# Kernel tuning notes

Measured on AMD Instinct MI355X. Metric: run time of the kernel, lower is better.

## Reference

```python
import jax, jax.numpy as jnp
import numpy as np

N_OPENIE = 100000
N_ENTITY = 100000
E = 150000
D_IN = 512
D_OUT = 512
H = 8
DH = D_OUT // H
NEG_SLOPE = 0.2


def setup_inputs() -> dict:
    key = jax.random.key(0)
    ks = jax.random.split(key, 16)
    def rn(k, shape, scale=0.05):
        return jax.random.normal(k, shape, dtype=jnp.float32) * scale
    return {
        "x_openie": jax.random.normal(ks[0], (N_OPENIE, D_IN), dtype=jnp.float32),
        "x_entity": jax.random.normal(ks[1], (N_ENTITY, D_IN), dtype=jnp.float32),
        "edge_e2o": jax.random.randint(ks[2], (2, E), 0, N_OPENIE, dtype=jnp.int32),
        "edge_o2o": jax.random.randint(ks[3], (2, E), 0, N_OPENIE, dtype=jnp.int32),
        "proj_o_w": rn(ks[4], (D_IN, D_OUT)),
        "proj_o_b": jnp.zeros((D_OUT,), jnp.float32),
        "proj_e_w": rn(ks[5], (D_IN, D_OUT)),
        "proj_e_b": jnp.zeros((D_OUT,), jnp.float32),
        "att_src_e2o": rn(ks[6], (H, DH)),
        "att_dst_e2o": rn(ks[7], (H, DH)),
        "att_src_o2o": rn(ks[8], (H, DH)),
        "att_dst_o2o": rn(ks[9], (H, DH)),
        "k_lin_w": rn(ks[10], (D_OUT, D_OUT)),
        "k_lin_b": jnp.zeros((D_OUT,), jnp.float32),
        "q_sem": rn(ks[11], (D_OUT,)),
        "lin_w": rn(ks[12], (D_OUT, 2)),
        "lin_b": jnp.zeros((2,), jnp.float32),
    }


def _edge_type_conv(h_src, h_dst, att_src, att_dst, src, dst, n_dst):
    # GAT-style per-edge-type attention (one metapath of HANConv).
    a_src = jnp.einsum('nhd,hd->nh', h_src, att_src)  # [N_src, H]
    a_dst = jnp.einsum('nhd,hd->nh', h_dst, att_dst)  # [N_dst, H]
    alpha = jax.nn.leaky_relu(a_src[src] + a_dst[dst], NEG_SLOPE)  # [E, H]
    amax = jax.ops.segment_max(alpha, dst, num_segments=n_dst)     # [N_dst, H]
    ex = jnp.exp(alpha - amax[dst])
    denom = jax.ops.segment_sum(ex, dst, num_segments=n_dst)
    w = ex / (denom[dst] + 1e-16)                                   # softmax over in-edges
    msg = h_src[src] * w[:, :, None]                                # [E, H, DH]
    out = jax.ops.segment_sum(msg, dst, num_segments=n_dst)        # [N_dst, H, DH]
    return jax.nn.relu(out.reshape(n_dst, H * DH))


def reference(x_openie, x_entity, edge_e2o, edge_o2o, proj_o_w, proj_o_b, proj_e_w,
              proj_e_b, att_src_e2o, att_dst_e2o, att_src_o2o, att_dst_o2o,
              k_lin_w, k_lin_b, q_sem, lin_w, lin_b):
    # Per-node-type projection to heads
    h_o = (x_openie @ proj_o_w + proj_o_b).reshape(-1, H, DH)
    h_e = (x_entity @ proj_e_w + proj_e_b).reshape(-1, H, DH)
    # Two metapaths ending at 'openie'
    out0 = _edge_type_conv(h_e, h_o, att_src_e2o, att_dst_e2o, edge_e2o[0], edge_e2o[1], N_OPENIE)
    out1 = _edge_type_conv(h_o, h_o, att_src_o2o, att_dst_o2o, edge_o2o[0], edge_o2o[1], N_OPENIE)
    # Semantic-level attention across metapaths
    outs = jnp.stack([out0, out1])                         # [M, N, F]
    k = jnp.tanh(outs @ k_lin_w + k_lin_b).mean(axis=1)    # [M, F]
    sem = jax.nn.softmax((k * q_sem).sum(-1))              # [M]
    fused = jnp.einsum('m,mnf->nf', sem, outs)             # [N, F]
    # global mean pool (single graph) -> dropout (eval: identity) -> Linear(F, 2)
    pooled = fused.mean(axis=0, keepdims=True)             # [1, F]
    return pooled @ lin_w + lin_b                          # [1, 2]
```

## Files before the change

### kernel.cpp

```cpp
#include <hip/hip_runtime.h>
#include <math.h>

#define N_NODES 100000
#define N_EDGES 150000
#define D 512
#define H 8
#define NEG_SLOPE 0.2f
#define NBR 782
#define NBLK (NBR * 4)

typedef __attribute__((ext_vector_type(8))) short bf16x8;
typedef __attribute__((ext_vector_type(4))) float f32x4;

__device__ __forceinline__ float bf2f(unsigned short u) { return __uint_as_float(((unsigned int)u) << 16); }
__device__ __forceinline__ unsigned short f2bf(float f) {
    unsigned int u = __float_as_uint(f);
    unsigned int r = u + 0x7FFFu + ((u >> 16) & 1u);
    return (unsigned short)(r >> 16);
}
__device__ __forceinline__ unsigned int pkbf(float a, float b) {
    unsigned int ua = __float_as_uint(a) + 0x8000u;
    unsigned int ub = __float_as_uint(b) + 0x8000u;
    return (ua >> 16) | (ub & 0xFFFF0000u);
}
__device__ __forceinline__ void gl_lds16(const void* g, void* l) {
    __builtin_amdgcn_global_load_lds((const __attribute__((address_space(1))) void*)g,
                                     (__attribute__((address_space(3))) void*)l, 16, 0, 0);
}
__device__ __forceinline__ float fast_tanh(float x) {
    float e = __expf(2.0f * x);
    float r;
    asm("v_rcp_f32 %0, %1" : "=v"(r) : "v"(e + 1.0f));
    return 1.0f - 2.0f * r;
}
__device__ __forceinline__ void map_block(int lin, int& rblk, int& cblk) {
    int g = lin >> 5;
    if (g < (NBR >> 3)) { rblk = g * 8 + (lin & 7); cblk = (lin >> 3) & 3; }
    else { int idx = lin - (NBR >> 3) * 32; rblk = (NBR & ~7) + (idx >> 2); cblk = idx & 3; }
}

__global__ __launch_bounds__(256)
void hist_edges(const int* __restrict__ e2o, const int* __restrict__ o2o, int* __restrict__ deg) {
    int i = blockIdx.x * 256 + threadIdx.x;
    if (i < N_EDGES) atomicAdd(&deg[e2o[N_EDGES + i]], 1);
    else if (i < 2 * N_EDGES) atomicAdd(&deg[N_NODES + o2o[N_EDGES + (i - N_EDGES)]], 1);
}

__global__ __launch_bounds__(256)
void scan1(const int* __restrict__ deg, int* __restrict__ rowptr, int* __restrict__ partials, int n) {
    __shared__ int lds[256];
    int t = threadIdx.x, b = blockIdx.x;
    int base = b * 1024 + t * 4;
    int d0 = (base + 0 < n) ? deg[base + 0] : 0;
    int d1 = (base + 1 < n) ? deg[base + 1] : 0;
    int d2 = (base + 2 < n) ? deg[base + 2] : 0;
    int d3 = (base + 3 < n) ? deg[base + 3] : 0;
    int s = d0 + d1 + d2 + d3;
    lds[t] = s;
    __syncthreads();
    for (int off = 1; off < 256; off <<= 1) {
        int v = (t >= off) ? lds[t - off] : 0;
        __syncthreads();
        lds[t] += v;
        __syncthreads();
    }
    int incl = lds[t];
    int eb = incl - s;
    if (base + 0 < n) rowptr[base + 0] = eb;
    if (base + 1 < n) rowptr[base + 1] = eb + d0;
    if (base + 2 < n) rowptr[base + 2] = eb + d0 + d1;
    if (base + 3 < n) rowptr[base + 3] = eb + d0 + d1 + d2;
    if (t == 255) partials[b] = incl;
}

__global__ __launch_bounds__(256)
void scan23(int* __restrict__ rowptr, const int* __restrict__ partials,
            int* __restrict__ cursor, int n, int total, int nb) {
    __shared__ int lds[256];
    int t = threadIdx.x, b = blockIdx.x;
    lds[t] = (t < nb) ? partials[t] : 0;
    __syncthreads();
    for (int off = 1; off < 256; off <<= 1) {
        int v = (t >= off) ? lds[t - off] : 0;
        __syncthreads();
        lds[t] += v;
        __syncthreads();
    }
    int add = (b == 0) ? 0 : lds[b - 1];
    int base = b * 1024 + t * 4;
    #pragma unroll
    for (int j = 0; j < 4; ++j) {
        if (base + j < n) {
            int v = rowptr[base + j] + add;
            rowptr[base + j] = v;
            cursor[base + j] = v;
        }
    }
    if (b == 0 && t == 0) rowptr[n] = total;
}

__global__ __launch_bounds__(256)
void fill_csr(const int* __restrict__ e2o, const int* __restrict__ o2o,
              int* __restrict__ cursor, int* __restrict__ csr) {
    int i = blockIdx.x * 256 + threadIdx.x;
    if (i < N_EDGES) {
        int d = e2o[N_EDGES + i];
        int p = atomicAdd(&cursor[d], 1);
        csr[p] = e2o[i];
    } else if (i < 2 * N_EDGES) {
        int j = i - N_EDGES;
        int d = o2o[N_EDGES + j];
        int p = atomicAdd(&cursor[N_NODES + d], 1);
        csr[p] = o2o[j];
    }
}

__global__ __launch_bounds__(256)
void transpose3(const float* __restrict__ W0, const float* __restrict__ W1, const float* __restrict__ W2,
                unsigned short* __restrict__ T0, unsigned short* __restrict__ T1, unsigned short* __restrict__ T2) {
    __shared__ float tile[32][33];
    int z = blockIdx.z;
    const float* W = (z == 0) ? W0 : (z == 1) ? W1 : W2;
    unsigned short* T = (z == 0) ? T0 : (z == 1) ? T1 : T2;
    int bx = blockIdx.x, by = blockIdx.y;
    int t = threadIdx.x, tx = t & 31, ty = t >> 5;
    #pragma unroll
    for (int p = 0; p < 4; ++p) {
        int k = by * 32 + ty + p * 8;
        tile[ty + p * 8][tx] = W[(size_t)k * D + bx * 32 + tx];
    }
    __syncthreads();
    #pragma unroll
    for (int p = 0; p < 4; ++p) {
        int n = bx * 32 + ty + p * 8;
        T[(size_t)n * D + by * 32 + tx] = f2bf(tile[tx][ty + p * 8]);
    }
}

__global__ __launch_bounds__(256)
void convert2(const float4* __restrict__ x0, const float4* __restrict__ x1,
              uint2* __restrict__ y0, uint2* __restrict__ y1) {
    const int n4 = N_NODES * D / 4;
    int i = blockIdx.x * 256 + threadIdx.x;
    const float4* s; uint2* d; int j;
    if (i < n4) { s = x0; d = y0; j = i; }
    else { s = x1; d = y1; j = i - n4; }
    float4 v = s[j];
    uint2 o; o.x = pkbf(v.x, v.y); o.y = pkbf(v.z, v.w);
    d[j] = o;
}

__global__ __launch_bounds__(256)
void gemm_proj2(const unsigned short* __restrict__ A0, const unsigned short* __restrict__ A1,
                const unsigned short* __restrict__ Bt0, const unsigned short* __restrict__ Bt1,
                const float* __restrict__ b0, const float* __restrict__ b1,
                unsigned short* __restrict__ C0, unsigned short* __restrict__ C1,
                const float* __restrict__ at00, const float* __restrict__ at01, const float* __restrict__ at02,
                float* __restrict__ ao00, float* __restrict__ ao01, float* __restrict__ ao02,
                const float* __restrict__ at10, float* __restrict__ ao10)
{
    __shared__ __align__(16) unsigned short As[2][4096];
    __shared__ __align__(16) unsigned short Bs[2][4096];
    const int M = N_NODES;
    int lin = blockIdx.x;
    int half = (lin >= NBLK) ? 1 : 0;
    lin -= half * NBLK;
    int rblk, cblk; map_block(lin, rblk, cblk);
    const unsigned short* A  = half ? A1 : A0;
    const unsigned short* Bt = half ? Bt1 : Bt0;
    const float* bias        = half ? b1 : b0;
    unsigned short* C        = half ? C1 : C0;
    const int natt = half ? 1 : 3;
    const float* attA = half ? at10 : at00;
    const float* attB = at01;
    const float* attC = at02;
    float* aoA = half ? ao10 : ao00;
    float* aoB = ao01;
    float* aoC = ao02;

    const int tid = threadIdx.x, lane = tid & 63, wave = tid >> 6;
    const int rb = rblk * 128, cb = cblk * 128;
    const int wm = (wave >> 1) * 64, wn = (wave & 1) * 64;

    const unsigned short* agp[2]; const unsigned short* bgp[2];
    #pragma unroll
    for (int c = 0; c < 2; ++c) {
        int s = wave * 2 + c;
        int rA = rb + s * 16 + (lane & 15); if (rA > M - 1) rA = M - 1;
        agp[c] = A + (size_t)rA * D + (lane >> 4) * 8;
        int rB = cb + s * 16 + (lane & 15);
        bgp[c] = Bt + (size_t)rB * D + (lane >> 4) * 8;
    }

    f32x4 acc[4][4];
    #pragma unroll
    for (int i = 0; i < 4; ++i)
        #pragma unroll
        for (int j = 0; j < 4; ++j) acc[i][j] = (f32x4){0.f, 0.f, 0.f, 0.f};

    #pragma unroll
    for (int c = 0; c < 2; ++c) {
        int s = wave * 2 + c;
        gl_lds16(agp[c], &As[0][s * 512]); agp[c] += 32;
        gl_lds16(bgp[c], &Bs[0][s * 512]); bgp[c] += 32;
    }
    __syncthreads();

    int buf = 0;
    for (int k = 0; k < 16; ++k) {
        if (k < 15) {
            #pragma unroll
            for (int c = 0; c < 2; ++c) {
                int s = wave * 2 + c;
                gl_lds16(agp[c], &As[buf ^ 1][s * 512]); agp[c] += 32;
                gl_lds16(bgp[c], &Bs[buf ^ 1][s * 512]); bgp[c] += 32;
            }
        }
        bf16x8 af[4], bfr[4];
        #pragma unroll
        for (int mi = 0; mi < 4; ++mi) af[mi] = *(const bf16x8*)&As[buf][((wave >> 1) * 4 + mi) * 512 + lane * 8];
        #pragma unroll
        for (int ni = 0; ni < 4; ++ni) bfr[ni] = *(const bf16x8*)&Bs[buf][((wave & 1) * 4 + ni) * 512 + lane * 8];
        #pragma unroll
        for (int mi = 0; mi < 4; ++mi)
            #pragma unroll
            for (int ni = 0; ni < 4; ++ni)
                acc[mi][ni] = __builtin_amdgcn_mfma_f32_16x16x32_bf16(af[mi], bfr[ni], acc[mi][ni], 0, 0, 0);
        __syncthreads();
        buf ^= 1;
    }

    float bb[4], av0[4], av1[4], av2[4];
    const int head = (cb + wn) >> 6;
    #pragma unroll
    for (int ni = 0; ni < 4; ++ni) {
        int ci = ni * 16 + (lane & 15);
        bb[ni] = bias[cb + wn + ci];
        av0[ni] = attA[head * 64 + ci];
        if (natt > 1) { av1[ni] = attB[head * 64 + ci]; av2[ni] = attC[head * 64 + ci]; }
    }
    #pragma unroll
    for (int mi = 0; mi < 4; ++mi) {
        #pragma unroll
        for (int r = 0; r < 4; ++r) {
            int rg = rb + wm + mi * 16 + (lane >> 4) * 4 + r;
            bool ok = rg < M;
            float v[4];
            #pragma unroll
            for (int ni = 0; ni < 4; ++ni) v[ni] = acc[mi][ni][r] + bb[ni];
            if (ok) {
                size_t base = (size_t)rg * D + cb + wn + (lane & 15);
                #pragma unroll
                for (int ni = 0; ni < 4; ++ni) C[base + ni * 16] = f2bf(v[ni]);
            }
            float s0 = v[0] * av0[0] + v[1] * av0[1] + v[2] * av0[2] + v[3] * av0[3];
            float s1 = 0.f, s2 = 0.f;
            if (natt > 1) {
                s1 = v[0] * av1[0] + v[1] * av1[1] + v[2] * av1[2] + v[3] * av1[3];
                s2 = v[0] * av2[0] + v[1] * av2[1] + v[2] * av2[2] + v[3] * av2[3];
            }
            #pragma unroll
            for (int m2 = 1; m2 < 16; m2 <<= 1) {
                s0 += __shfl_xor(s0, m2);
                if (natt > 1) { s1 += __shfl_xor(s1, m2); s2 += __shfl_xor(s2, m2); }
            }
            if (ok && (lane & 15) == 0) {
                aoA[rg * H + head] = s0;
                if (natt > 1) { aoB[rg * H + head] = s1; aoC[rg * H + head] = s2; }
            }
        }
    }
}

__global__ __launch_bounds__(256)
void aggregate2(const int* __restrict__ rowptr, const int* __restrict__ csr,
                const float* __restrict__ aS0, const float* __restrict__ aD0, const unsigned short* __restrict__ hE,
                const float* __restrict__ aS1, const float* __restrict__ aD1, const unsigned short* __restrict__ hO,
                unsigned short* __restrict__ out0, unsigned short* __restrict__ out1)
{
    int gw = (blockIdx.x * 256 + threadIdx.x) >> 6;
    int lane = threadIdx.x & 63;
    if (gw >= 2 * N_NODES) return;
    int half = gw >= N_NODES;
    int node = gw - half * N_NODES;
    const float* a_src = half ? aS1 : aS0;
    const float* a_dst = half ? aD1 : aD0;
    const unsigned short* h = half ? hO : hE;
    unsigned short* out = half ? out1 : out0;

    int beg = rowptr[gw], end = rowptr[gw + 1];
    int hh = lane & 7;
    float adst = a_dst[node * H + hh];

    float amax = -1e30f;
    for (int p = beg; p < end; ++p) {
        int s = csr[p];
        float al = a_src[s * H + hh] + adst;
        al = (al >= 0.f) ? al : NEG_SLOPE * al;
        amax = fmaxf(amax, al);
    }
    float denom = 0.f;
    for (int p = beg; p < end; ++p) {
        int s = csr[p];
        float al = a_src[s * H + hh] + adst;
        al = (al >= 0.f) ? al : NEG_SLOPE * al;
        denom += expf(al - amax);
    }
    float inv = 1.f / (denom + 1e-16f);

    float acc[8] = {0.f, 0.f, 0.f, 0.f, 0.f, 0.f, 0.f, 0.f};
    for (int p = beg; p < end; ++p) {
        int s = csr[p];
        float al = a_src[s * H + hh] + adst;
        al = (al >= 0.f) ? al : NEG_SLOPE * al;
        float w = expf(al - amax) * inv;
        const unsigned short* hp = h + (size_t)s * D;
        #pragma unroll
        for (int h2 = 0; h2 < 8; ++h2) {
            float wh = __shfl(w, h2);
            acc[h2] += bf2f(hp[h2 * 64 + lane]) * wh;
        }
    }
    size_t base = (size_t)node * D;
    #pragma unroll
    for (int h2 = 0; h2 < 8; ++h2)
        out[base + h2 * 64 + lane] = f2bf(fmaxf(acc[h2], 0.f));
}

__global__ __launch_bounds__(256)
void colsum2(const unsigned short* __restrict__ ob0, const unsigned short* __restrict__ ob1,
             float* __restrict__ colsum)
{
    __shared__ float red[512];
    int b = blockIdx.x;
    int half = b >= NBR;
    const unsigned short* ob = half ? ob1 : ob0;
    float* cs = colsum + half * 512;
    int t = threadIdx.x;
    int r0 = (b - half * NBR) * 128;
    int c8 = t & 63;
    float s[8] = {0.f, 0.f, 0.f, 0.f, 0.f, 0.f, 0.f, 0.f};
    for (int it = 0; it < 32; ++it) {
        int row = r0 + it * 4 + (t >> 6);
        if (row < N_NODES) {
            uint4 v = *((const uint4*)(ob + (size_t)row * D) + c8);
            s[0] += bf2f((unsigned short)(v.x & 0xFFFF)); s[1] += bf2f((unsigned short)(v.x >> 16));
            s[2] += bf2f((unsigned short)(v.y & 0xFFFF)); s[3] += bf2f((unsigned short)(v.y >> 16));
            s[4] += bf2f((unsigned short)(v.z & 0xFFFF)); s[5] += bf2f((unsigned short)(v.z >> 16));
            s[6] += bf2f((unsigned short)(v.w & 0xFFFF)); s[7] += bf2f((unsigned short)(v.w >> 16));
        }
    }
    red[t] = 0.f; red[t + 256] = 0.f;
    __syncthreads();
    #pragma unroll
    for (int j = 0; j < 8; ++j) atomicAdd(&red[c8 * 8 + j], s[j]);
    __syncthreads();
    atomicAdd(&cs[t & 511], red[t]);
    atomicAdd(&cs[(t + 256) & 511], red[t + 256]);
}

__global__ __launch_bounds__(256)
void gemm_tanh2(const unsigned short* __restrict__ Ah0, const unsigned short* __restrict__ Ah1,
                const unsigned short* __restrict__ Bt, const float* __restrict__ bias,
                float* __restrict__ ksum)
{
    __shared__ __align__(16) unsigned short As[2][4096];
    __shared__ __align__(16) unsigned short Bs[2][4096];
    const int M = N_NODES;
    int lin = blockIdx.x;
    int half = (lin >= NBLK) ? 1 : 0;
    lin -= half * NBLK;
    int rblk, cblk; map_block(lin, rblk, cblk);
    const unsigned short* A = half ? Ah1 : Ah0;
    float* ks = ksum + half * 512;

    const int tid = threadIdx.x, lane = tid & 63, wave = tid >> 6;
    const int rb = rblk * 128, cb = cblk * 128;
    const int wm = (wave >> 1) * 64, wn = (wave & 1) * 64;

    const unsigned short* agp[2]; const unsigned short* bgp[2];
    #pragma unroll
    for (int c = 0; c < 2; ++c) {
        int s = wave * 2 + c;
        int rA = rb + s * 16 + (lane & 15); if (rA > M - 1) rA = M - 1;
        agp[c] = A + (size_t)rA * D + (lane >> 4) * 8;
        int rB = cb + s * 16 + (lane & 15);
        bgp[c] = Bt + (size_t)rB * D + (lane >> 4) * 8;
    }

    f32x4 acc[4][4];
    #pragma unroll
    for (int i = 0; i < 4; ++i)
        #pragma unroll
        for (int j = 0; j < 4; ++j) acc[i][j] = (f32x4){0.f, 0.f, 0.f, 0.f};

    #pragma unroll
    for (int c = 0; c < 2; ++c) {
        int s = wave * 2 + c;
        gl_lds16(agp[c], &As[0][s * 512]); agp[c] += 32;
        gl_lds16(bgp[c], &Bs[0][s * 512]); bgp[c] += 32;
    }
    __syncthreads();

    int buf = 0;
    for (int k = 0; k < 16; ++k) {
        if (k < 15) {
            #pragma unroll
            for (int c = 0; c < 2; ++c) {
                int s = wave * 2 + c;
                gl_lds16(agp[c], &As[buf ^ 1][s * 512]); agp[c] += 32;
                gl_lds16(bgp[c], &Bs[buf ^ 1][s * 512]); bgp[c] += 32;
            }
        }
        bf16x8 af[4], bfr[4];
        #pragma unroll
        for (int mi = 0; mi < 4; ++mi) af[mi] = *(const bf16x8*)&As[buf][((wave >> 1) * 4 + mi) * 512 + lane * 8];
        #pragma unroll
        for (int ni = 0; ni < 4; ++ni) bfr[ni] = *(const bf16x8*)&Bs[buf][((wave & 1) * 4 + ni) * 512 + lane * 8];
        #pragma unroll
        for (int mi = 0; mi < 4; ++mi)
            #pragma unroll
            for (int ni = 0; ni < 4; ++ni)
                acc[mi][ni] = __builtin_amdgcn_mfma_f32_16x16x32_bf16(af[mi], bfr[ni], acc[mi][ni], 0, 0, 0);
        __syncthreads();
        buf ^= 1;
    }

    float bb[4];
    #pragma unroll
    for (int ni = 0; ni < 4; ++ni) bb[ni] = bias[cb + wn + ni * 16 + (lane & 15)];
    float cs[4] = {0.f, 0.f, 0.f, 0.f};
    #pragma unroll
    for (int mi = 0; mi < 4; ++mi) {
        #pragma unroll
        for (int r = 0; r < 4; ++r) {
            int rg = rb + wm + mi * 16 + (lane >> 4) * 4 + r;
            if (rg < M) {
                #pragma unroll
                for (int ni = 0; ni < 4; ++ni)
                    cs[ni] += fast_tanh(acc[mi][ni][r] + bb[ni]);
            }
        }
    }
    __syncthreads();
    float* red = (float*)As;
    if (tid < 128) red[tid] = 0.f;
    __syncthreads();
    #pragma unroll
    for (int ni = 0; ni < 4; ++ni) atomicAdd(&red[wn + ni * 16 + (lane & 15)], cs[ni]);
    __syncthreads();
    if (tid < 128) atomicAdd(&ks[cb + tid], red[tid]);
}

__global__ __launch_bounds__(256)
void finalize(const float* __restrict__ ksum, const float* __restrict__ colsum,
              const float* __restrict__ q_sem, const float* __restrict__ lin_w,
              const float* __restrict__ lin_b, float* __restrict__ dout)
{
    __shared__ float red[256];
    __shared__ float semsh[2];
    int t = threadIdx.x;
    const float invN = 1.0f / (float)N_NODES;
    float p0 = ksum[t] * q_sem[t] + ksum[t + 256] * q_sem[t + 256];
    float p1 = ksum[512 + t] * q_sem[t] + ksum[512 + t + 256] * q_sem[t + 256];

    red[t] = p0; __syncthreads();
    for (int s = 128; s > 0; s >>= 1) { if (t < s) red[t] += red[t + s]; __syncthreads(); }
    float S0 = red[0]; __syncthreads();
    red[t] = p1; __syncthreads();
    for (int s = 128; s > 0; s >>= 1) { if (t < s) red[t] += red[t + s]; __syncthreads(); }
    float S1 = red[0]; __syncthreads();

    if (t == 0) {
        float a0 = S0 * invN, a1 = S1 * invN;
        float mx = fmaxf(a0, a1);
        float e0 = expf(a0 - mx), e1 = expf(a1 - mx);
        semsh[0] = e0 / (e0 + e1);
        semsh[1] = e1 / (e0 + e1);
    }
    __syncthreads();
    float sem0 = semsh[0], sem1 = semsh[1];

    float o0 = 0.f, o1 = 0.f;
    #pragma unroll
    for (int q = 0; q < 2; ++q) {
        int f = t + q * 256;
        float pooled = (sem0 * colsum[f] + sem1 * colsum[512 + f]) * invN;
        o0 += pooled * lin_w[f * 2 + 0];
        o1 += pooled * lin_w[f * 2 + 1];
    }
    red[t] = o0; __syncthreads();
    for (int s = 128; s > 0; s >>= 1) { if (t < s) red[t] += red[t + s]; __syncthreads(); }
    if (t == 0) dout[0] = red[0] + lin_b[0];
    __syncthreads();
    red[t] = o1; __syncthreads();
    for (int s = 128; s > 0; s >>= 1) { if (t < s) red[t] += red[t + s]; __syncthreads(); }
    if (t == 0) dout[1] = red[0] + lin_b[1];
}

extern "C" void kernel_launch(void* const* d_in, const int* in_sizes, int n_in,
                              void* d_out, int out_size, void* d_ws, size_t ws_size,
                              hipStream_t stream)
{
    const float* x_o    = (const float*)d_in[0];
    const float* x_e    = (const float*)d_in[1];
    const int*   e2o    = (const int*)d_in[2];
    const int*   o2o    = (const int*)d_in[3];
    const float* pow_   = (const float*)d_in[4];
    const float* pob    = (const float*)d_in[5];
    const float* pew    = (const float*)d_in[6];
    const float* peb    = (const float*)d_in[7];
    const float* as_e2o = (const float*)d_in[8];
    const float* ad_e2o = (const float*)d_in[9];
    const float* as_o2o = (const float*)d_in[10];
    const float* ad_o2o = (const float*)d_in[11];
    const float* klw    = (const float*)d_in[12];
    const float* klb    = (const float*)d_in[13];
    const float* qsem   = (const float*)d_in[14];
    const float* linw   = (const float*)d_in[15];
    const float* linb   = (const float*)d_in[16];

    char* ws = (char*)d_ws;
    size_t off = 0;
    auto alloc = [&](size_t bytes) { void* p = ws + off; off += (bytes + 255) & ~(size_t)255; return p; };

    unsigned short* xbf_o = (unsigned short*)alloc((size_t)N_NODES * D * 2);
    unsigned short* xbf_e = (unsigned short*)alloc((size_t)N_NODES * D * 2);
    unsigned short* h_o   = (unsigned short*)alloc((size_t)N_NODES * D * 2);
    unsigned short* h_e   = (unsigned short*)alloc((size_t)N_NODES * D * 2);
    unsigned short* obf0  = (unsigned short*)alloc((size_t)N_NODES * D * 2);
    unsigned short* obf1  = (unsigned short*)alloc((size_t)N_NODES * D * 2);
    unsigned short* wt_po = (unsigned short*)alloc((size_t)D * D * 2);
    unsigned short* wt_pe = (unsigned short*)alloc((size_t)D * D * 2);
    unsigned short* wt_kl = (unsigned short*)alloc((size_t)D * D * 2);
    float* aS0 = (float*)alloc((size_t)N_NODES * H * 4);
    float* aD0 = (float*)alloc((size_t)N_NODES * H * 4);
    float* aS1 = (float*)alloc((size_t)N_NODES * H * 4);
    float* aD1 = (float*)alloc((size_t)N_NODES * H * 4);
    int* misc    = (int*)alloc((2048 + 2 * N_NODES) * 4);
    float* colsum = (float*)misc;
    float* ksum   = colsum + 1024;
    int* deg      = misc + 2048;
    int* cursor  = (int*)alloc(2 * N_NODES * 4);
    int* rowptr  = (int*)alloc((2 * N_NODES + 1) * 4);
    int* partials= (int*)alloc(256 * 4);
    int* csr     = (int*)alloc(2 * N_EDGES * 4);

    const int NSC = 2 * N_NODES;
    const int NB1 = (NSC + 1023) / 1024;
    const int EH  = (2 * N_EDGES + 255) / 256;

    hipMemsetAsync(misc, 0, (size_t)(2048 + 2 * N_NODES) * 4, stream);

    hist_edges<<<EH, 256, 0, stream>>>(e2o, o2o, deg);
    scan1<<<NB1, 256, 0, stream>>>(deg, rowptr, partials, NSC);
    scan23<<<NB1, 256, 0, stream>>>(rowptr, partials, cursor, NSC, 2 * N_EDGES, NB1);
    fill_csr<<<EH, 256, 0, stream>>>(e2o, o2o, cursor, csr);

    transpose3<<<dim3(16, 16, 3), 256, 0, stream>>>(pow_, pew, klw, wt_po, wt_pe, wt_kl);
    convert2<<<(2 * N_NODES * D / 4) / 256, 256, 0, stream>>>(
        (const float4*)x_o, (const float4*)x_e, (uint2*)xbf_o, (uint2*)xbf_e);

    gemm_proj2<<<2 * NBLK, 256, 0, stream>>>(
        xbf_o, xbf_e, wt_po, wt_pe, pob, peb, h_o, h_e,
        ad_e2o, as_o2o, ad_o2o, aD0, aS1, aD1,
        as_e2o, aS0);

    aggregate2<<<(2 * N_NODES * 64) / 256, 256, 0, stream>>>(
        rowptr, csr, aS0, aD0, h_e, aS1, aD1, h_o, obf0, obf1);
    colsum2<<<2 * NBR, 256, 0, stream>>>(obf0, obf1, colsum);
    gemm_tanh2<<<2 * NBLK, 256, 0, stream>>>(obf0, obf1, wt_kl, klb, ksum);

    finalize<<<1, 256, 0, stream>>>(ksum, colsum, qsem, linw, linb, (float*)d_out);
}
```

Baseline: 1.211 ms.

## Triple-buffer LDS in projection and tanh GEMMs with partial vmcnt waits

Both bf16 MFMA GEMM kernels move from a double-buffered LDS pipeline to a three-stage ring, prefetching two K-tiles ahead. The full __syncthreads is replaced by explicit s_waitcnt vmcnt(4) plus s_barrier, so only the oldest tile's loads must complete. This is meant to hide global-load latency behind MFMA work. In exchange, LDS use per block grows from 32KB to 48KB, which may lower occupancy, and correctness now depends on hand-counted vmcnt values.

```diff
diff --git a/kernel.cpp b/kernel.cpp
--- a/kernel.cpp
+++ b/kernel.cpp
@@ -159,8 +159,8 @@
                 float* __restrict__ ao00, float* __restrict__ ao01, float* __restrict__ ao02,
                 const float* __restrict__ at10, float* __restrict__ ao10)
 {
-    __shared__ __align__(16) unsigned short As[2][4096];
-    __shared__ __align__(16) unsigned short Bs[2][4096];
+    __shared__ __align__(16) unsigned short As[3][4096];
+    __shared__ __align__(16) unsigned short Bs[3][4096];
     const int M = N_NODES;
     int lin = blockIdx.x;
     int half = (lin >= NBLK) ? 1 : 0;
@@ -183,9 +183,11 @@
     const int wm = (wave >> 1) * 64, wn = (wave & 1) * 64;
 
     const unsigned short* agp[2]; const unsigned short* bgp[2];
+    int sub[2];
     #pragma unroll
     for (int c = 0; c < 2; ++c) {
         int s = wave * 2 + c;
+        sub[c] = s;
         int rA = rb + s * 16 + (lane & 15); if (rA > M - 1) rA = M - 1;
         agp[c] = A + (size_t)rA * D + (lane >> 4) * 8;
         int rB = cb + s * 16 + (lane & 15);
@@ -200,34 +202,46 @@
 
     #pragma unroll
     for (int c = 0; c < 2; ++c) {
-        int s = wave * 2 + c;
-        gl_lds16(agp[c], &As[0][s * 512]); agp[c] += 32;
-        gl_lds16(bgp[c], &Bs[0][s * 512]); bgp[c] += 32;
-    }
-    __syncthreads();
-
-    int buf = 0;
+        gl_lds16(agp[c], &As[0][sub[c] * 512]); agp[c] += 32;
+        gl_lds16(bgp[c], &Bs[0][sub[c] * 512]); bgp[c] += 32;
+    }
+    #pragma unroll
+    for (int c = 0; c < 2; ++c) {
+        gl_lds16(agp[c], &As[1][sub[c] * 512]); agp[c] += 32;
+        gl_lds16(bgp[c], &Bs[1][sub[c] * 512]); bgp[c] += 32;
+    }
+    asm volatile("s_waitcnt vmcnt(4)" ::: "memory");
+    __builtin_amdgcn_s_barrier();
+
+    unsigned short *aR = As[0], *bR = Bs[0];
+    unsigned short *aM = As[1], *bM = Bs[1];
+    unsigned short *aP = As[2], *bP = Bs[2];
+
     for (int k = 0; k < 16; ++k) {
-        if (k < 15) {
+        bf16x8 af[4], bfr[4];
+        #pragma unroll
+        for (int mi = 0; mi < 4; ++mi) af[mi] = *(const bf16x8*)&aR[((wave >> 1) * 4 + mi) * 512 + lane * 8];
+        #pragma unroll
+        for (int ni = 0; ni < 4; ++ni) bfr[ni] = *(const bf16x8*)&bR[((wave & 1) * 4 + ni) * 512 + lane * 8];
+        if (k < 14) {
             #pragma unroll
             for (int c = 0; c < 2; ++c) {
-                int s = wave * 2 + c;
-                gl_lds16(agp[c], &As[buf ^ 1][s * 512]); agp[c] += 32;
-                gl_lds16(bgp[c], &Bs[buf ^ 1][s * 512]); bgp[c] += 32;
+                gl_lds16(agp[c], &aP[sub[c] * 512]); agp[c] += 32;
+                gl_lds16(bgp[c], &bP[sub[c] * 512]); bgp[c] += 32;
             }
         }
-        bf16x8 af[4], bfr[4];
-        #pragma unroll
-        for (int mi = 0; mi < 4; ++mi) af[mi] = *(const bf16x8*)&As[buf][((wave >> 1) * 4 + mi) * 512 + lane * 8];
-        #pragma unroll
-        for (int ni = 0; ni < 4; ++ni) bfr[ni] = *(const bf16x8*)&Bs[buf][((wave & 1) * 4 + ni) * 512 + lane * 8];
         #pragma unroll
         for (int mi = 0; mi < 4; ++mi)
             #pragma unroll
             for (int ni = 0; ni < 4; ++ni)
                 acc[mi][ni] = __builtin_amdgcn_mfma_f32_16x16x32_bf16(af[mi], bfr[ni], acc[mi][ni], 0, 0, 0);
-        __syncthreads();
-        buf ^= 1;
+        __builtin_amdgcn_sched_barrier(0);
+        if (k < 14) asm volatile("s_waitcnt vmcnt(4) lgkmcnt(0)" ::: "memory");
+        else        asm volatile("s_waitcnt vmcnt(0) lgkmcnt(0)" ::: "memory");
+        __builtin_amdgcn_s_barrier();
+        unsigned short* t;
+        t = aR; aR = aM; aM = aP; aP = t;
+        t = bR; bR = bM; bM = bP; bP = t;
     }
 
     float bb[4], av0[4], av1[4], av2[4];
@@ -364,8 +378,8 @@
                 const unsigned short* __restrict__ Bt, const float* __restrict__ bias,
                 float* __restrict__ ksum)
 {
-    __shared__ __align__(16) unsigned short As[2][4096];
-    __shared__ __align__(16) unsigned short Bs[2][4096];
+    __shared__ __align__(16) unsigned short As[3][4096];
+    __shared__ __align__(16) unsigned short Bs[3][4096];
     const int M = N_NODES;
     int lin = blockIdx.x;
     int half = (lin >= NBLK) ? 1 : 0;
@@ -379,9 +393,11 @@
     const int wm = (wave >> 1) * 64, wn = (wave & 1) * 64;
 
     const unsigned short* agp[2]; const unsigned short* bgp[2];
+    int sub[2];
     #pragma unroll
     for (int c = 0; c < 2; ++c) {
         int s = wave * 2 + c;
+        sub[c] = s;
         int rA = rb + s * 16 + (lane & 15); if (rA > M - 1) rA = M - 1;
         agp[c] = A + (size_t)rA * D + (lane >> 4) * 8;
         int rB = cb + s * 16 + (lane & 15);
@@ -396,34 +412,46 @@
 
     #pragma unroll
     for (int c = 0; c < 2; ++c) {
-        int s = wave * 2 + c;
-        gl_lds16(agp[c], &As[0][s * 512]); agp[c] += 32;
-        gl_lds16(bgp[c], &Bs[0][s * 512]); bgp[c] += 32;
-    }
-    __syncthreads();
-
-    int buf = 0;
+        gl_lds16(agp[c], &As[0][sub[c] * 512]); agp[c] += 32;
+        gl_lds16(bgp[c], &Bs[0][sub[c] * 512]); bgp[c] += 32;
+    }
+    #pragma unroll
+    for (int c = 0; c < 2; ++c) {
+        gl_lds16(agp[c], &As[1][sub[c] * 512]); agp[c] += 32;
+        gl_lds16(bgp[c], &Bs[1][sub[c] * 512]); bgp[c] += 32;
+    }
+    asm volatile("s_waitcnt vmcnt(4)" ::: "memory");
+    __builtin_amdgcn_s_barrier();
+
+    unsigned short *aR = As[0], *bR = Bs[0];
+    unsigned short *aM = As[1], *bM = Bs[1];
+    unsigned short *aP = As[2], *bP = Bs[2];
+
     for (int k = 0; k < 16; ++k) {
-        if (k < 15) {
+        bf16x8 af[4], bfr[4];
+        #pragma unroll
+        for (int mi = 0; mi < 4; ++mi) af[mi] = *(const bf16x8*)&aR[((wave >> 1) * 4 + mi) * 512 + lane * 8];
+        #pragma unroll
+        for (int ni = 0; ni < 4; ++ni) bfr[ni] = *(const bf16x8*)&bR[((wave & 1) * 4 + ni) * 512 + lane * 8];
+        if (k < 14) {
             #pragma unroll
             for (int c = 0; c < 2; ++c) {
-                int s = wave * 2 + c;
-                gl_lds16(agp[c], &As[buf ^ 1][s * 512]); agp[c] += 32;
-                gl_lds16(bgp[c], &Bs[buf ^ 1][s * 512]); bgp[c] += 32;
+                gl_lds16(agp[c], &aP[sub[c] * 512]); agp[c] += 32;
+                gl_lds16(bgp[c], &bP[sub[c] * 512]); bgp[c] += 32;
             }
         }
-        bf16x8 af[4], bfr[4];
-        #pragma unroll
-        for (int mi = 0; mi < 4; ++mi) af[mi] = *(const bf16x8*)&As[buf][((wave >> 1) * 4 + mi) * 512 + lane * 8];
-        #pragma unroll
-        for (int ni = 0; ni < 4; ++ni) bfr[ni] = *(const bf16x8*)&Bs[buf][((wave & 1) * 4 + ni) * 512 + lane * 8];
         #pragma unroll
         for (int mi = 0; mi < 4; ++mi)
             #pragma unroll
             for (int ni = 0; ni < 4; ++ni)
                 acc[mi][ni] = __builtin_amdgcn_mfma_f32_16x16x32_bf16(af[mi], bfr[ni], acc[mi][ni], 0, 0, 0);
-        __syncthreads();
-        buf ^= 1;
+        __builtin_amdgcn_sched_barrier(0);
+        if (k < 14) asm volatile("s_waitcnt vmcnt(4) lgkmcnt(0)" ::: "memory");
+        else        asm volatile("s_waitcnt vmcnt(0) lgkmcnt(0)" ::: "memory");
+        __builtin_amdgcn_s_barrier();
+        unsigned short* t;
+        t = aR; aR = aM; aM = aP; aP = t;
+        t = bR; bR = bM; bM = bP; bP = t;
     }
 
     float bb[4];
```

After: 1.187 ms. -2.0%, faster.
